# Optimization experiments

Hardware: AMD Instinct MI355X
Metric: run time of the kernel (lower is better)

Reference implementation:

```python
import jax, jax.numpy as jnp
import numpy as np
from jax import lax

PATCH = 15
WIDTH_DCP = 55


def _box_sum(x, r):
    # AvgPool2d(kernel=2r+1, stride=1, padding=r, count_include_pad=True) * (2r+1)^2;
    # the kernel-size factor cancels in all mean_*/N ratios below.
    return lax.reduce_window(x, 0.0, lax.add, (1, 1, 2 * r + 1, 2 * r + 1),
                             (1, 1, 1, 1), ((0, 0), (0, 0), (r, r), (r, r)))


def _guided_filter(I, p, r, eps):
    Nn = _box_sum(jnp.ones_like(p), r)
    mean_I = _box_sum(I, r) / Nn
    mean_p = _box_sum(p, r) / Nn
    mean_Ip = _box_sum(I * p, r) / Nn
    cov_Ip = mean_Ip - mean_I * mean_p
    mean_II = _box_sum(I * I, r) / Nn
    var_I = mean_II - mean_I * mean_I
    a = cov_Ip / (var_I + eps)
    b = mean_p - a * mean_I
    mean_a = _box_sum(a, r) / Nn
    mean_b = _box_sum(b, r) / Nn
    return mean_a * I + mean_b


def _dark_channel(x):
    d = x.min(axis=1, keepdims=True)
    pad = WIDTH_DCP // 2
    d = jnp.pad(d, ((0, 0), (0, 0), (pad, pad), (pad, pad)), constant_values=1.0)
    return lax.reduce_window(d, jnp.inf, lax.min, (1, 1, WIDTH_DCP, WIDTH_DCP),
                             (1, 1, 1, 1), 'VALID')


def _map_A(x):
    N, C, H, W = x.shape
    dc = _dark_channel(x).reshape(N, -1)
    k = int(H * W * 0.001)
    _, idx = lax.top_k(dc, k)  # brightest dark-channel pixels
    xr = x.reshape(N, 3, -1)
    searched = jnp.take_along_axis(xr, jnp.broadcast_to(idx[:, None, :], (N, 3, k)), axis=2)
    A = searched.mean(axis=2)
    return jnp.broadcast_to(A[:, :, None, None], x.shape)


def _t_bccr(haze, mapA, ps):
    t1 = (mapA - haze) / (mapA - 20.0 / 255.0)
    t2 = (mapA - haze) / (mapA - 300.0 / 255.0)
    t = jnp.maximum(t1, t2).max(axis=1, keepdims=True)
    pad = ps // 2
    t = jnp.pad(t, ((0, 0), (0, 0), (pad, pad), (pad, pad)), constant_values=0.0)
    t = lax.reduce_window(t, -jnp.inf, lax.max, (1, 1, ps, ps), (1, 1, 1, 1), 'VALID')
    return jnp.clip(t, 0.05, 1.0)


def _pad_reshape(data, ps):
    N, C, H, W = data.shape
    pad_H = (ps - H % ps) % ps
    pad_W = (ps - W % ps) % ps
    padded = jnp.pad(data, ((0, 0), (0, 0), (pad_H // 2, pad_H - pad_H // 2),
                            (pad_W // 2, pad_W - pad_W // 2)), mode='edge')
    nH = padded.shape[2] // ps
    nW = padded.shape[3] // ps
    p = padded[:, 0].reshape(N, nH, ps, nW, ps).transpose(0, 1, 3, 2, 4)
    p = p.reshape(N, nH * nW, ps * ps).transpose(0, 2, 1)  # [N, ps*ps, P]
    return p, pad_H // 2, pad_W // 2, nH, nW


def _transmission(S, V1, ps, pixel_number=10, slp_length=0.1):
    X, sH, sW, nH, nW = _pad_reshape(V1, ps)  # [N, pp, P]
    Y, _, _, _, _ = _pad_reshape(S, ps)
    dX = X[:, :, None, :] - X[:, None, :, :]          # [N, pp, pp, P]
    dY = Y[:, :, None, :] - Y[:, None, :, :]
    slope = dY / (dX + 1e-8)
    smask = ((slope > -1) & (slope < 0)).astype(X.dtype)
    scount = smask.sum(axis=2)                         # [N, pp, P]
    pmask = (scount >= 0.5 * ps * ps).astype(X.dtype)
    pcount = pmask.sum(axis=1, keepdims=True)          # [N, 1, P]
    mx = (X * pmask).sum(axis=1, keepdims=True) / (pcount + 1e-5)
    my = (Y * pmask).sum(axis=1, keepdims=True) / (pcount + 1e-5)
    k = ((X * Y * pmask).sum(axis=1, keepdims=True) - pcount * mx * my) / (
        ((X * pmask) ** 2).sum(axis=1, keepdims=True) - pcount * mx ** 2 + 1e-5)
    b = my - k * mx
    t = 1.0 + k / (b + 1e-8)
    length = (1.0 + k ** 2) ** 0.5 * ((X * pmask).max(axis=1, keepdims=True)
                                      - (X + 1e8 * (1.0 - pmask)).min(axis=1, keepdims=True))
    tmask = ((pcount > pixel_number) & (length > slp_length) & (k > -1) & (k < 0)
             & (t > 0.01) & (t < 1 - 0.01)).astype(X.dtype)
    t = (t * tmask).reshape(-1, 1, nH, nW)
    t = jnp.repeat(jnp.repeat(t, ps, axis=2), ps, axis=3)  # nearest upsample x ps
    return t[:, :, sH:S.shape[2] + sH, sW:S.shape[3] + sW]


def _percentile(t, bili=0.05):
    N = t.shape[0]
    flat = jnp.where(t > 0, t, 10.0).reshape(N, -1)
    s = jnp.sort(flat, axis=1)
    n = flat.shape[1]
    idx = min(int(bili * n), n - 1)
    return s[:, idx].reshape(-1, 1, 1, 1)


def _restore(image, ps=PATCH):
    mapA = _map_A(image)
    norm = image / mapA
    mx = norm.max(axis=1, keepdims=True)
    S = 1.0 - norm.min(axis=1, keepdims=True) / (mx + 1e-8)
    V1 = 1.0 / (mx + 1e-8)
    t1 = _transmission(S, V1, ps)
    half = ps // 2
    t2 = _transmission(S[:, :, half:, half:], V1[:, :, half:, half:], ps)
    t2 = jnp.pad(t2, ((0, 0), (0, 0), (half, 0), (half, 0)), constant_values=0.0)
    t_slp = jnp.where((t1 != 0) & (t2 != 0), (t1 + t2) / 2.0,
                      jnp.where(t1 != 0, t1, t2))
    t_bl = _t_bccr(image, mapA, ps)
    t_min = _percentile(t_slp)
    t_fusion = jnp.clip(jnp.where(t_slp > 0, t_slp, t_bl), t_min, 1.0)
    t_ref = _guided_filter(image.mean(axis=1, keepdims=True), t_fusion, 2 * ps, 1e-3)
    return (image - mapA) / t_ref + mapA


def setup_inputs() -> dict:
    key = jax.random.key(0)
    image = jax.random.uniform(key, (1, 3, 480, 480), dtype=jnp.float32)
    return {"image": image}


def reference(image):
    return _restore(image)
```

## Files before the change

### kernel.cpp

```cpp
#include <hip/hip_runtime.h>
#include <math.h>

#define W 480
#define HT 480
#define HW (W*HT)
#define GE (HW/256)
#define PP 225
#define NPATCH 1024
#define EQCAP 8192

struct State {
  unsigned slotP[4];
  unsigned slotK[4];
  float sumA[3];
  unsigned eqCount;
  float A[3];
  unsigned tminbits;
  unsigned eqIdx[EQCAP];
  float tp1[NPATCH];
  float tp2[NPATCH];
};

__device__ __forceinline__ void resolve_level(const unsigned* __restrict__ h,
                                              unsigned k_in, int desc,
                                              unsigned* lds,
                                              unsigned& chosen, unsigned& k_out) {
  int t = threadIdx.x;
  unsigned c = h[desc ? (255 - t) : t];
  lds[t] = c;
  __syncthreads();
  for (int s = 1; s < 256; s <<= 1) {
    unsigned add = (t >= s) ? lds[t - s] : 0u;
    __syncthreads();
    lds[t] += add;
    __syncthreads();
  }
  unsigned incl = lds[t];
  unsigned excl = incl - c;
  if (incl >= k_in && excl < k_in) { lds[256] = (unsigned)t; lds[257] = k_in - excl; }
  __syncthreads();
  unsigned tt = lds[256];
  k_out = lds[257];
  chosen = desc ? (255u - tt) : tt;
  __syncthreads();
}

__global__ __launch_bounds__(512) void k_rowmin(const float* __restrict__ img,
                                                float* __restrict__ rowmin,
                                                State* st, unsigned* __restrict__ hist16) {
  __shared__ float l[534];
  int y = blockIdx.x, t = threadIdx.x;
  int g = y * 512 + t;
  if (g < 65536) hist16[g] = 0u;
  for (int i = t; i < 534; i += 512) {
    int col = i - 27;
    float v = 1.0f;
    if ((unsigned)col < (unsigned)W) {
      int q = y * W + col;
      v = fminf(fminf(img[q], img[HW + q]), img[2 * HW + q]);
    }
    l[i] = v;
  }
  if (g == 0) { st->sumA[0] = 0.f; st->sumA[1] = 0.f; st->sumA[2] = 0.f; st->eqCount = 0u; }
  __syncthreads();
  if (t < W) {
    float m = l[t];
    for (int d = 1; d < 55; ++d) m = fminf(m, l[t + d]);
    rowmin[y * W + t] = m;
  }
}

__global__ __launch_bounds__(256) void k_minV3(const float* __restrict__ rowmin,
                                               float* __restrict__ dc,
                                               unsigned* __restrict__ hist16) {
  __shared__ unsigned short bs[256];
  int t = threadIdx.x;
  int p = blockIdx.x * 256 + t;
  int y = p / W, x = p - y * W;
  int lo = y - 27, hi = y + 27;
  float m = (lo < 0 || hi >= HT) ? 1.0f : INFINITY;
  int lo2 = max(lo, 0), hi2 = min(hi, HT - 1);
  for (int yy = lo2; yy <= hi2; ++yy) m = fminf(m, rowmin[yy * W + x]);
  dc[p] = m;
  unsigned b16 = __float_as_uint(m) >> 16;
  bs[t] = (unsigned short)b16;
  __syncthreads();
  int firstIdx = 256, cnt = 0;
  for (int j = 0; j < 256; ++j) {
    if ((unsigned)bs[j] == b16) { ++cnt; if (j < firstIdx) firstIdx = j; }
  }
  if (firstIdx == t) atomicAdd(&hist16[b16], (unsigned)cnt);
}

__global__ __launch_bounds__(256) void k_resolve16(const unsigned* __restrict__ hist16,
                                                   State* st) {
  __shared__ unsigned lds[258];
  __shared__ unsigned lh[256];
  int t = threadIdx.x;
  const uint4* h4 = (const uint4*)hist16;
  unsigned s = 0;
  for (int i = 0; i < 64; ++i) { uint4 v = h4[t * 64 + i]; s += v.x + v.y + v.z + v.w; }
  lh[t] = s;
  __syncthreads();
  unsigned ct, kc;
  resolve_level(lh, 230u, 1, lds, ct, kc);
  lh[t] = hist16[ct * 256 + t];
  __syncthreads();
  unsigned b, kp;
  resolve_level(lh, kc, 1, lds, b, kp);
  if (t == 0) { st->slotP[0] = (ct << 8) | b; st->slotK[0] = kp; }
}

__global__ __launch_bounds__(256) void k_gather2(const float* __restrict__ dc,
                                                 const float* __restrict__ img, State* st) {
  __shared__ float ls[3];
  __shared__ unsigned lcnt, lbase;
  int t = threadIdx.x;
  if (t == 0) { ls[0] = 0.f; ls[1] = 0.f; ls[2] = 0.f; lcnt = 0u; }
  __syncthreads();
  int p = blockIdx.x * 256 + t;
  unsigned p16 = st->slotP[0];
  unsigned b16 = __float_as_uint(dc[p]) >> 16;
  bool eq = (b16 == p16);
  unsigned my = 0;
  if (b16 > p16) {
    atomicAdd(&ls[0], img[p]);
    atomicAdd(&ls[1], img[HW + p]);
    atomicAdd(&ls[2], img[2 * HW + p]);
  } else if (eq) {
    my = atomicAdd(&lcnt, 1u);
  }
  __syncthreads();
  if (t == 0 && lcnt) lbase = atomicAdd(&st->eqCount, lcnt);
  __syncthreads();
  if (eq) { unsigned pos = lbase + my; if (pos < (unsigned)EQCAP) st->eqIdx[pos] = (unsigned)p; }
  if (t == 0 && (ls[0] != 0.f || ls[1] != 0.f || ls[2] != 0.f)) {
    atomicAdd(&st->sumA[0], ls[0]);
    atomicAdd(&st->sumA[1], ls[1]);
    atomicAdd(&st->sumA[2], ls[2]);
  }
}

__global__ __launch_bounds__(256) void k_finalizeA2(const float* __restrict__ dc,
                                                    const float* __restrict__ img, State* st) {
  __shared__ unsigned lds[258];
  __shared__ unsigned lh[256];
  __shared__ unsigned sIdx[EQCAP];
  __shared__ unsigned short sVal[EQCAP];
  __shared__ float ssum[3];
  int t = threadIdx.x;
  unsigned k = st->slotK[0];
  unsigned ne = st->eqCount; if (ne > (unsigned)EQCAP) ne = EQCAP;
  for (int i = t; i < (int)ne; i += 256) {
    unsigned q = st->eqIdx[i];
    sIdx[i] = q;
    sVal[i] = (unsigned short)(__float_as_uint(dc[q]) & 0xFFFFu);
  }
  if (t < 3) ssum[t] = 0.f;
  __syncthreads();
  unsigned vpfx = 0u;
  for (int lev = 0; lev < 2; ++lev) {
    int s = 8 - 8 * lev;
    lh[t] = 0u;
    __syncthreads();
    for (int i = t; i < (int)ne; i += 256) {
      unsigned v = (unsigned)sVal[i];
      if (lev == 0 || (v >> 8) == (vpfx >> 8))
        atomicAdd(&lh[(v >> s) & 0xFFu], 1u);
    }
    __syncthreads();
    unsigned ch, kn;
    resolve_level(lh, k, 1, lds, ch, kn);
    vpfx |= ch << s;
    k = kn;
  }
  unsigned pfx = 0u;
  for (int lev = 0; lev < 3; ++lev) {
    int s = 16 - 8 * lev;
    lh[t] = 0u;
    __syncthreads();
    for (int i = t; i < (int)ne; i += 256) {
      if ((unsigned)sVal[i] == vpfx) {
        unsigned v = sIdx[i];
        if ((v >> (s + 8)) == (pfx >> (s + 8)))
          atomicAdd(&lh[(v >> s) & 0xFFu], 1u);
      }
    }
    __syncthreads();
    unsigned ch, kn;
    resolve_level(lh, k, 0, lds, ch, kn);
    pfx |= ch << s;
    k = kn;
  }
  float a0 = 0.f, a1 = 0.f, a2 = 0.f;
  for (int i = t; i < (int)ne; i += 256) {
    unsigned v = (unsigned)sVal[i], q = sIdx[i];
    if (v > vpfx || (v == vpfx && q <= pfx)) {
      a0 += img[q]; a1 += img[HW + q]; a2 += img[2 * HW + q];
    }
  }
  atomicAdd(&ssum[0], a0); atomicAdd(&ssum[1], a1); atomicAdd(&ssum[2], a2);
  __syncthreads();
  if (t == 0) {
    st->A[0] = (st->sumA[0] + ssum[0]) / 230.0f;
    st->A[1] = (st->sumA[1] + ssum[1]) / 230.0f;
    st->A[2] = (st->sumA[2] + ssum[2]) / 230.0f;
  }
}

__device__ __forceinline__ float wred_sum(float v) { for (int m = 32; m; m >>= 1) v += __shfl_xor(v, m, 64); return v; }
__device__ __forceinline__ float wred_max(float v) { for (int m = 32; m; m >>= 1) v = fmaxf(v, __shfl_xor(v, m, 64)); return v; }
__device__ __forceinline__ float wred_min(float v) { for (int m = 32; m; m >>= 1) v = fminf(v, __shfl_xor(v, m, 64)); return v; }

__global__ __launch_bounds__(256) void k_mega1(const float* __restrict__ img,
                                               float* __restrict__ mh, State* st) {
  __shared__ float2 XY[PP];
  __shared__ float part[4][8];
  __shared__ float Tl[494];
  int b = blockIdx.x;
  int t = threadIdx.x;
  float A0 = st->A[0], A1 = st->A[1], A2 = st->A[2];
  const float c20 = (float)(20.0 / 255.0);
  const float c300 = (float)(300.0 / 255.0);
  if (b >= 2048) {
    int y = b - 2048;
    for (int i = t; i < 494; i += 256) {
      int col = i - 7;
      float v = 0.0f;
      if ((unsigned)col < (unsigned)W) {
        int q = y * W + col;
        float r = img[q], g = img[HW + q], bl = img[2 * HW + q];
        float t0 = fmaxf((A0 - r) / (A0 - c20), (A0 - r) / (A0 - c300));
        float t1 = fmaxf((A1 - g) / (A1 - c20), (A1 - g) / (A1 - c300));
        float t2 = fmaxf((A2 - bl) / (A2 - c20), (A2 - bl) / (A2 - c300));
        v = fmaxf(fmaxf(t0, t1), t2);
      }
      Tl[i] = v;
    }
    __syncthreads();
    for (int x = t; x < W; x += 256) {
      float m = -INFINITY;
      for (int d = 0; d < 15; ++d) m = fmaxf(m, Tl[x + d]);
      mh[y * W + x] = m;
    }
    return;
  }
  int mode = b >> 10;
  int pid = b & 1023;
  int ph = pid >> 5, pw = pid & 31;
  if (t < PP) {
    int r = t / 15, c = t - (t / 15) * 15;
    int y, x;
    if (mode == 0) { y = ph * 15 + r; x = pw * 15 + c; }
    else {
      y = ph * 15 + r + 4; y = (y < 7) ? 7 : ((y > 479) ? 479 : y);
      x = pw * 15 + c + 4; x = (x < 7) ? 7 : ((x > 479) ? 479 : x);
    }
    int q = y * W + x;
    float rr = img[q], gg = img[HW + q], bb = img[2 * HW + q];
    float nr = rr / A0, ng = gg / A1, nb = bb / A2;
    float mx = fmaxf(fmaxf(nr, ng), nb);
    float mn = fminf(fminf(nr, ng), nb);
    float d = mx + 1e-8f;
    XY[t] = make_float2(1.0f / d, 1.0f - mn / d);
  }
  __syncthreads();
  float xi = 0.f, yi = 0.f;
  int cnt = 0;
  if (t < PP) {
    xi = XY[t].x; yi = XY[t].y;
    #pragma unroll 5
    for (int j = 0; j < PP; ++j) {
      float2 o = XY[j];
      float dY = yi - o.y;
      float D = (xi - o.x) + 1e-8f;
      cnt += ((dY * D < 0.0f) && (fabsf(dY) < fabsf(D))) ? 1 : 0;
    }
  }
  float pmf = (t < PP && cnt >= 113) ? 1.0f : 0.0f;
  float xm = xi * pmf, ym = yi * pmf;
  float v0 = wred_sum(pmf);
  float v1 = wred_sum(xm);
  float v2 = wred_sum(ym);
  float v3 = wred_sum(xm * ym);
  float v4 = wred_sum(xm * xm);
  float v5 = wred_max((t < PP) ? xm : -INFINITY);
  float v6 = wred_min((t < PP) ? (xi + 1e8f * (1.0f - pmf)) : INFINITY);
  int wid = t >> 6, lane = t & 63;
  if (lane == 0) {
    part[wid][0] = v0; part[wid][1] = v1; part[wid][2] = v2; part[wid][3] = v3;
    part[wid][4] = v4; part[wid][5] = v5; part[wid][6] = v6;
  }
  __syncthreads();
  if (t == 0) {
    float pcount = 0.f, sx = 0.f, sy = 0.f, sxy = 0.f, sxx = 0.f;
    float mxX = -INFINITY, mnX = INFINITY;
    for (int w2 = 0; w2 < 4; ++w2) {
      pcount += part[w2][0]; sx += part[w2][1]; sy += part[w2][2];
      sxy += part[w2][3]; sxx += part[w2][4];
      mxX = fmaxf(mxX, part[w2][5]); mnX = fminf(mnX, part[w2][6]);
    }
    float den = pcount + 1e-5f;
    float mxv = sx / den, myv = sy / den;
    float kk = (sxy - pcount * mxv * myv) / (sxx - pcount * (mxv * mxv) + 1e-5f);
    float bb = myv - kk * mxv;
    float tt = 1.0f + kk / (bb + 1e-8f);
    float len = sqrtf(1.0f + kk * kk) * (mxX - mnX);
    bool m = (pcount > 10.0f) && (len > 0.1f) && (kk > -1.0f) && (kk < 0.0f)
             && (tt > 0.01f) && (tt < 0.99f);
    float res = tt * (m ? 1.0f : 0.0f);
    if (mode == 0) st->tp1[pid] = res; else st->tp2[pid] = res;
  }
}

__global__ __launch_bounds__(256) void k_maxV_pct(const float* __restrict__ mh,
                                                  float* __restrict__ tb, State* st) {
  __shared__ unsigned lh[256];
  __shared__ unsigned lds[258];
  __shared__ float tp1s[NPATCH], tp2s[NPATCH];
  int b = blockIdx.x;
  int t = threadIdx.x;
  if (b < GE) {
    int p = b * 256 + t;
    int y = p / W, x = p - y * W;
    float m = -INFINITY;
    for (int d = -7; d <= 7; ++d) {
      int yy = y + d;
      float v = ((unsigned)yy < (unsigned)HT) ? mh[yy * W + x] : 0.0f;
      m = fmaxf(m, v);
    }
    tb[p] = fminf(fmaxf(m, 0.05f), 1.0f);
    return;
  }
  for (int i = t; i < NPATCH; i += 256) { tp1s[i] = st->tp1[i]; tp2s[i] = st->tp2[i]; }
  __syncthreads();
  unsigned prefix = 0u, k = 11521u;
  for (int level = 0; level < 4; ++level) {
    lh[t] = 0u;
    __syncthreads();
    unsigned mask = (level == 0) ? 0u : (0xFFFFFFFFu << (32 - 8 * level));
    int shift = 24 - 8 * level;
    for (int i = t; i < NPATCH; i += 256) {
      int ph = i >> 5, pw = i & 31;
      float a = tp1s[i];
      int rcnt[2], ridx[2], ccnt[2], cidx[2];
      if (ph == 0) { rcnt[0] = 7; ridx[0] = -1; rcnt[1] = 8; ridx[1] = 0; }
      else         { rcnt[0] = 4; ridx[0] = ph - 1; rcnt[1] = 11; ridx[1] = ph; }
      if (pw == 0) { ccnt[0] = 7; cidx[0] = -1; ccnt[1] = 8; cidx[1] = 0; }
      else         { ccnt[0] = 4; cidx[0] = pw - 1; ccnt[1] = 11; cidx[1] = pw; }
      for (int ri = 0; ri < 2; ++ri)
        for (int ci = 0; ci < 2; ++ci) {
          unsigned area = (unsigned)(rcnt[ri] * ccnt[ci]);
          float bb = 0.0f;
          if (ridx[ri] >= 0 && cidx[ci] >= 0) bb = tp2s[ridx[ri] * 32 + cidx[ci]];
          float r;
          if (a != 0.0f && bb != 0.0f) r = (a + bb) / 2.0f;
          else r = (a != 0.0f) ? a : bb;
          float u = (r > 0.0f) ? r : 10.0f;
          unsigned bits = __float_as_uint(u);
          if ((bits & mask) == prefix)
            atomicAdd(&lh[(bits >> shift) & 0xFFu], area);
        }
    }
    __syncthreads();
    unsigned ch, kn;
    resolve_level(lh, k, 0, lds, ch, kn);
    prefix |= ch << shift;
    k = kn;
  }
  if (t == 0) st->tminbits = prefix;
}

__global__ __launch_bounds__(512) void k_gf1h(const float* __restrict__ img,
                                              const float* __restrict__ tb,
                                              const State* __restrict__ st,
                                              float4* __restrict__ box4) {
  __shared__ float tp1s[NPATCH], tp2s[NPATCH];
  __shared__ float Pl[540], Il[540];
  int y = blockIdx.x, t = threadIdx.x;
  for (int i = t; i < NPATCH; i += 512) { tp1s[i] = st->tp1[i]; tp2s[i] = st->tp2[i]; }
  __syncthreads();
  float tmin = __uint_as_float(st->tminbits);
  int c1row = (y / 15) * 32;
  bool c2ok = (y >= 7);
  int c2row = c2ok ? ((y - 4) / 15) * 32 : 0;
  for (int i = t; i < 540; i += 512) {
    int col = i - 30;
    float pv = 0.0f, iv = 0.0f;
    if ((unsigned)col < (unsigned)W) {
      int q = y * W + col;
      float a = tp1s[c1row + col / 15];
      float bb = 0.0f;
      if (c2ok && col >= 7) bb = tp2s[c2row + (col - 4) / 15];
      float r;
      if (a != 0.0f && bb != 0.0f) r = (a + bb) / 2.0f;
      else r = (a != 0.0f) ? a : bb;
      float v = (r > 0.0f) ? r : tb[q];
      v = (v < tmin) ? tmin : v;
      v = (v > 1.0f) ? 1.0f : v;
      pv = v;
      iv = ((img[q] + img[HW + q]) + img[2 * HW + q]) / 3.0f;
    }
    Pl[i] = pv; Il[i] = iv;
  }
  __syncthreads();
  if (t < W) {
    float sI = 0.f, sP = 0.f, sIp = 0.f, sII = 0.f;
    for (int d = 0; d < 61; ++d) {
      float iv = Il[t + d], pv = Pl[t + d];
      sI += iv; sP += pv; sIp += iv * pv; sII += iv * iv;
    }
    box4[y * W + t] = make_float4(sI, sP, sIp, sII);
  }
}

__global__ __launch_bounds__(512) void k_gf1vh(const float4* __restrict__ box4,
                                               float2* __restrict__ hab) {
  __shared__ float2 l[540];
  int y = blockIdx.x, t = threadIdx.x;
  float2 v = make_float2(0.f, 0.f);
  if (t < W) {
    float sI = 0.f, sP = 0.f, sIp = 0.f, sII = 0.f;
    for (int d = -30; d <= 30; ++d) {
      int yy = y + d;
      if ((unsigned)yy < (unsigned)HT) {
        float4 b = box4[yy * W + t];
        sI += b.x; sP += b.y; sIp += b.z; sII += b.w;
      }
    }
    int ny = min(y + 30, HT - 1) - max(y - 30, 0) + 1;
    int nx = min(t + 30, W - 1) - max(t - 30, 0) + 1;
    float Nn = (float)(ny * nx);
    float mI = sI / Nn, mP = sP / Nn, mIp = sIp / Nn, mII = sII / Nn;
    float cov = mIp - mI * mP;
    float var = mII - mI * mI;
    float av = cov / (var + 1e-3f);
    v = make_float2(av, mP - av * mI);
  }
  if (t < 30) { l[t] = make_float2(0.f, 0.f); l[510 + t] = make_float2(0.f, 0.f); }
  if (t < W) l[30 + t] = v;
  __syncthreads();
  if (t < W) {
    float sa = 0.f, sb = 0.f;
    for (int d = 0; d < 61; ++d) { float2 u = l[t + d]; sa += u.x; sb += u.y; }
    hab[y * W + t] = make_float2(sa, sb);
  }
}

__global__ __launch_bounds__(256) void k_gf2vfin(const float2* __restrict__ hab,
                                                 const float* __restrict__ img,
                                                 const State* __restrict__ st,
                                                 float* __restrict__ out) {
  int p = blockIdx.x * 256 + threadIdx.x;
  int y = p / W, x = p - y * W;
  float sa = 0.f, sb = 0.f;
  for (int d = -30; d <= 30; ++d) {
    int yy = y + d;
    if ((unsigned)yy < (unsigned)HT) { float2 v = hab[yy * W + x]; sa += v.x; sb += v.y; }
  }
  int ny = min(y + 30, HT - 1) - max(y - 30, 0) + 1;
  int nx = min(x + 30, W - 1) - max(x - 30, 0) + 1;
  float Nn = (float)(ny * nx);
  float r = img[p], g = img[HW + p], bl = img[2 * HW + p];
  float Iv = ((r + g) + bl) / 3.0f;
  float tref = (sa / Nn) * Iv + (sb / Nn);
  float A0 = st->A[0], A1 = st->A[1], A2 = st->A[2];
  out[p]          = (r  - A0) / tref + A0;
  out[HW + p]     = (g  - A1) / tref + A1;
  out[2 * HW + p] = (bl - A2) / tref + A2;
}

extern "C" void kernel_launch(void* const* d_in, const int* in_sizes, int n_in,
                              void* d_out, int out_size, void* d_ws, size_t ws_size,
                              hipStream_t stream) {
  (void)in_sizes; (void)n_in; (void)out_size; (void)ws_size;
  const float* img = (const float*)d_in[0];
  float* out = (float*)d_out;
  State* st = (State*)d_ws;
  unsigned* hist16 = (unsigned*)((char*)d_ws + 65536);
  float* sb = (float*)((char*)d_ws + 65536 + 262144);
  float* bufA = sb;
  float* bufB = sb + HW;
  float4* box4 = (float4*)(sb + 2 * HW);
  float2* hab  = (float2*)(sb + 6 * HW);

  dim3 b256(256), b512(512);
  dim3 ge(GE), rows(HT);

  k_rowmin<<<rows, b512, 0, stream>>>(img, bufB, st, hist16);
  k_minV3<<<ge, b256, 0, stream>>>(bufB, bufA, hist16);
  k_resolve16<<<dim3(1), b256, 0, stream>>>(hist16, st);
  k_gather2<<<ge, b256, 0, stream>>>(bufA, img, st);
  k_finalizeA2<<<dim3(1), b256, 0, stream>>>(bufA, img, st);
  k_mega1<<<dim3(2048 + HT), b256, 0, stream>>>(img, bufB, st);
  k_maxV_pct<<<dim3(GE + 1), b256, 0, stream>>>(bufB, bufA, st);
  k_gf1h<<<rows, b512, 0, stream>>>(img, bufA, st, box4);
  k_gf1vh<<<rows, b512, 0, stream>>>(box4, hab);
  k_gf2vfin<<<ge, b256, 0, stream>>>(hab, img, st, out);
}
```

Measured before the change: 185.5 us.

## Fold single-block resolve kernels into last-block-done tails and fuse vertical max

```diff
diff --git a/kernel.cpp b/kernel.cpp
--- a/kernel.cpp
+++ b/kernel.cpp
@@ -4,7 +4,7 @@
 #define W 480
 #define HT 480
 #define HW (W*HT)
-#define GE (HW/256)
+#define NT (HW/256)
 #define PP 225
 #define NPATCH 1024
 #define EQCAP 8192
@@ -16,6 +16,7 @@
   unsigned eqCount;
   float A[3];
   unsigned tminbits;
+  unsigned done1, done2, done3, pad0;
   unsigned eqIdx[EQCAP];
   float tp1[NPATCH];
   float tp2[NPATCH];
@@ -44,6 +45,10 @@
   chosen = desc ? (255u - tt) : tt;
   __syncthreads();
 }
+
+__device__ __forceinline__ float wred_sum(float v) { for (int m = 32; m; m >>= 1) v += __shfl_xor(v, m, 64); return v; }
+__device__ __forceinline__ float wred_max(float v) { for (int m = 32; m; m >>= 1) v = fmaxf(v, __shfl_xor(v, m, 64)); return v; }
+__device__ __forceinline__ float wred_min(float v) { for (int m = 32; m; m >>= 1) v = fminf(v, __shfl_xor(v, m, 64)); return v; }
 
 __global__ __launch_bounds__(512) void k_rowmin(const float* __restrict__ img,
                                                 float* __restrict__ rowmin,
@@ -61,7 +66,10 @@
     }
     l[i] = v;
   }
-  if (g == 0) { st->sumA[0] = 0.f; st->sumA[1] = 0.f; st->sumA[2] = 0.f; st->eqCount = 0u; }
+  if (g == 0) {
+    st->sumA[0] = 0.f; st->sumA[1] = 0.f; st->sumA[2] = 0.f; st->eqCount = 0u;
+    st->done1 = 0u; st->done2 = 0u; st->done3 = 0u;
+  }
   __syncthreads();
   if (t < W) {
     float m = l[t];
@@ -72,8 +80,11 @@
 
 __global__ __launch_bounds__(256) void k_minV3(const float* __restrict__ rowmin,
                                                float* __restrict__ dc,
-                                               unsigned* __restrict__ hist16) {
+                                               unsigned* __restrict__ hist16, State* st) {
   __shared__ unsigned short bs[256];
+  __shared__ unsigned s_lds[258];
+  __shared__ unsigned s_lh[256];
+  __shared__ unsigned isLast;
   int t = threadIdx.x;
   int p = blockIdx.x * 256 + t;
   int y = p / W, x = p - y * W;
@@ -90,31 +101,39 @@
     if ((unsigned)bs[j] == b16) { ++cnt; if (j < firstIdx) firstIdx = j; }
   }
   if (firstIdx == t) atomicAdd(&hist16[b16], (unsigned)cnt);
-}
-
-__global__ __launch_bounds__(256) void k_resolve16(const unsigned* __restrict__ hist16,
-                                                   State* st) {
-  __shared__ unsigned lds[258];
-  __shared__ unsigned lh[256];
-  int t = threadIdx.x;
-  const uint4* h4 = (const uint4*)hist16;
-  unsigned s = 0;
-  for (int i = 0; i < 64; ++i) { uint4 v = h4[t * 64 + i]; s += v.x + v.y + v.z + v.w; }
-  lh[t] = s;
-  __syncthreads();
-  unsigned ct, kc;
-  resolve_level(lh, 230u, 1, lds, ct, kc);
-  lh[t] = hist16[ct * 256 + t];
-  __syncthreads();
-  unsigned b, kp;
-  resolve_level(lh, kc, 1, lds, b, kp);
-  if (t == 0) { st->slotP[0] = (ct << 8) | b; st->slotK[0] = kp; }
+  if (t == 0) {
+    __threadfence();
+    unsigned old = atomicAdd(&st->done1, 1u);
+    isLast = (old == (unsigned)(NT - 1)) ? 1u : 0u;
+  }
+  __syncthreads();
+  if (isLast) {
+    __threadfence();
+    const uint4* h4 = (const uint4*)hist16;
+    unsigned s = 0;
+    for (int i = 0; i < 64; ++i) { uint4 v = h4[t * 64 + i]; s += v.x + v.y + v.z + v.w; }
+    s_lh[t] = s;
+    __syncthreads();
+    unsigned ct, kc;
+    resolve_level(s_lh, 230u, 1, s_lds, ct, kc);
+    s_lh[t] = hist16[ct * 256 + t];
+    __syncthreads();
+    unsigned b, kp;
+    resolve_level(s_lh, kc, 1, s_lds, b, kp);
+    if (t == 0) { st->slotP[0] = (ct << 8) | b; st->slotK[0] = kp; }
+  }
 }
 
 __global__ __launch_bounds__(256) void k_gather2(const float* __restrict__ dc,
                                                  const float* __restrict__ img, State* st) {
   __shared__ float ls[3];
   __shared__ unsigned lcnt, lbase;
+  __shared__ unsigned isLast;
+  __shared__ unsigned s_lds[258];
+  __shared__ unsigned s_lh[256];
+  __shared__ unsigned sIdx[EQCAP];
+  __shared__ unsigned short sVal[EQCAP];
+  __shared__ float ssum[3];
   int t = threadIdx.x;
   if (t == 0) { ls[0] = 0.f; ls[1] = 0.f; ls[2] = 0.f; lcnt = 0u; }
   __syncthreads();
@@ -139,84 +158,83 @@
     atomicAdd(&st->sumA[1], ls[1]);
     atomicAdd(&st->sumA[2], ls[2]);
   }
-}
-
-__global__ __launch_bounds__(256) void k_finalizeA2(const float* __restrict__ dc,
-                                                    const float* __restrict__ img, State* st) {
-  __shared__ unsigned lds[258];
-  __shared__ unsigned lh[256];
-  __shared__ unsigned sIdx[EQCAP];
-  __shared__ unsigned short sVal[EQCAP];
-  __shared__ float ssum[3];
-  int t = threadIdx.x;
-  unsigned k = st->slotK[0];
-  unsigned ne = st->eqCount; if (ne > (unsigned)EQCAP) ne = EQCAP;
-  for (int i = t; i < (int)ne; i += 256) {
-    unsigned q = st->eqIdx[i];
-    sIdx[i] = q;
-    sVal[i] = (unsigned short)(__float_as_uint(dc[q]) & 0xFFFFu);
-  }
-  if (t < 3) ssum[t] = 0.f;
-  __syncthreads();
-  unsigned vpfx = 0u;
-  for (int lev = 0; lev < 2; ++lev) {
-    int s = 8 - 8 * lev;
-    lh[t] = 0u;
-    __syncthreads();
+  if (t == 0) {
+    __threadfence();
+    unsigned old = atomicAdd(&st->done2, 1u);
+    isLast = (old == (unsigned)(NT - 1)) ? 1u : 0u;
+  }
+  __syncthreads();
+  if (isLast) {
+    __threadfence();
+    unsigned k = st->slotK[0];
+    unsigned ne = st->eqCount; if (ne > (unsigned)EQCAP) ne = EQCAP;
     for (int i = t; i < (int)ne; i += 256) {
-      unsigned v = (unsigned)sVal[i];
-      if (lev == 0 || (v >> 8) == (vpfx >> 8))
-        atomicAdd(&lh[(v >> s) & 0xFFu], 1u);
-    }
-    __syncthreads();
-    unsigned ch, kn;
-    resolve_level(lh, k, 1, lds, ch, kn);
-    vpfx |= ch << s;
-    k = kn;
-  }
-  unsigned pfx = 0u;
-  for (int lev = 0; lev < 3; ++lev) {
-    int s = 16 - 8 * lev;
-    lh[t] = 0u;
-    __syncthreads();
+      unsigned q = st->eqIdx[i];
+      sIdx[i] = q;
+      sVal[i] = (unsigned short)(__float_as_uint(dc[q]) & 0xFFFFu);
+    }
+    if (t < 3) ssum[t] = 0.f;
+    __syncthreads();
+    unsigned vpfx = 0u;
+    for (int lev = 0; lev < 2; ++lev) {
+      int s = 8 - 8 * lev;
+      s_lh[t] = 0u;
+      __syncthreads();
+      for (int i = t; i < (int)ne; i += 256) {
+        unsigned v = (unsigned)sVal[i];
+        if (lev == 0 || (v >> 8) == (vpfx >> 8))
+          atomicAdd(&s_lh[(v >> s) & 0xFFu], 1u);
+      }
+      __syncthreads();
+      unsigned ch, kn;
+      resolve_level(s_lh, k, 1, s_lds, ch, kn);
+      vpfx |= ch << s;
+      k = kn;
+    }
+    unsigned pfx = 0u;
+    for (int lev = 0; lev < 3; ++lev) {
+      int s = 16 - 8 * lev;
+      s_lh[t] = 0u;
+      __syncthreads();
+      for (int i = t; i < (int)ne; i += 256) {
+        if ((unsigned)sVal[i] == vpfx) {
+          unsigned v = sIdx[i];
+          if ((v >> (s + 8)) == (pfx >> (s + 8)))
+            atomicAdd(&s_lh[(v >> s) & 0xFFu], 1u);
+        }
+      }
+      __syncthreads();
+      unsigned ch, kn;
+      resolve_level(s_lh, k, 0, s_lds, ch, kn);
+      pfx |= ch << s;
+      k = kn;
+    }
+    float a0 = 0.f, a1 = 0.f, a2 = 0.f;
     for (int i = t; i < (int)ne; i += 256) {
-      if ((unsigned)sVal[i] == vpfx) {
-        unsigned v = sIdx[i];
-        if ((v >> (s + 8)) == (pfx >> (s + 8)))
-          atomicAdd(&lh[(v >> s) & 0xFFu], 1u);
+      unsigned v = (unsigned)sVal[i], q = sIdx[i];
+      if (v > vpfx || (v == vpfx && q <= pfx)) {
+        a0 += img[q]; a1 += img[HW + q]; a2 += img[2 * HW + q];
       }
     }
-    __syncthreads();
-    unsigned ch, kn;
-    resolve_level(lh, k, 0, lds, ch, kn);
-    pfx |= ch << s;
-    k = kn;
-  }
-  float a0 = 0.f, a1 = 0.f, a2 = 0.f;
-  for (int i = t; i < (int)ne; i += 256) {
-    unsigned v = (unsigned)sVal[i], q = sIdx[i];
-    if (v > vpfx || (v == vpfx && q <= pfx)) {
-      a0 += img[q]; a1 += img[HW + q]; a2 += img[2 * HW + q];
-    }
-  }
-  atomicAdd(&ssum[0], a0); atomicAdd(&ssum[1], a1); atomicAdd(&ssum[2], a2);
-  __syncthreads();
-  if (t == 0) {
-    st->A[0] = (st->sumA[0] + ssum[0]) / 230.0f;
-    st->A[1] = (st->sumA[1] + ssum[1]) / 230.0f;
-    st->A[2] = (st->sumA[2] + ssum[2]) / 230.0f;
-  }
-}
-
-__device__ __forceinline__ float wred_sum(float v) { for (int m = 32; m; m >>= 1) v += __shfl_xor(v, m, 64); return v; }
-__device__ __forceinline__ float wred_max(float v) { for (int m = 32; m; m >>= 1) v = fmaxf(v, __shfl_xor(v, m, 64)); return v; }
-__device__ __forceinline__ float wred_min(float v) { for (int m = 32; m; m >>= 1) v = fminf(v, __shfl_xor(v, m, 64)); return v; }
+    atomicAdd(&ssum[0], a0); atomicAdd(&ssum[1], a1); atomicAdd(&ssum[2], a2);
+    __syncthreads();
+    if (t == 0) {
+      st->A[0] = (st->sumA[0] + ssum[0]) / 230.0f;
+      st->A[1] = (st->sumA[1] + ssum[1]) / 230.0f;
+      st->A[2] = (st->sumA[2] + ssum[2]) / 230.0f;
+    }
+  }
+}
 
 __global__ __launch_bounds__(256) void k_mega1(const float* __restrict__ img,
                                                float* __restrict__ mh, State* st) {
   __shared__ float2 XY[PP];
   __shared__ float part[4][8];
   __shared__ float Tl[494];
+  __shared__ unsigned isLast;
+  __shared__ unsigned s_lds[258];
+  __shared__ unsigned s_lh[256];
+  __shared__ float tp1s[NPATCH], tp2s[NPATCH];
   int b = blockIdx.x;
   int t = threadIdx.x;
   float A0 = st->A[0], A1 = st->A[1], A2 = st->A[2];
@@ -311,74 +329,72 @@
     float res = tt * (m ? 1.0f : 0.0f);
     if (mode == 0) st->tp1[pid] = res; else st->tp2[pid] = res;
   }
-}
-
-__global__ __launch_bounds__(256) void k_maxV_pct(const float* __restrict__ mh,
-                                                  float* __restrict__ tb, State* st) {
-  __shared__ unsigned lh[256];
-  __shared__ unsigned lds[258];
+  if (t == 0) {
+    __threadfence();
+    unsigned old = atomicAdd(&st->done3, 1u);
+    isLast = (old == 2047u) ? 1u : 0u;
+  }
+  __syncthreads();
+  if (isLast) {
+    __threadfence();
+    for (int i = t; i < NPATCH; i += 256) { tp1s[i] = st->tp1[i]; tp2s[i] = st->tp2[i]; }
+    __syncthreads();
+    unsigned prefix = 0u, k = 11521u;
+    for (int level = 0; level < 4; ++level) {
+      s_lh[t] = 0u;
+      __syncthreads();
+      unsigned mask = (level == 0) ? 0u : (0xFFFFFFFFu << (32 - 8 * level));
+      int shift = 24 - 8 * level;
+      for (int i = t; i < NPATCH; i += 256) {
+        int phh = i >> 5, pww = i & 31;
+        float a = tp1s[i];
+        int rcnt[2], ridx[2], ccnt[2], cidx[2];
+        if (phh == 0) { rcnt[0] = 7; ridx[0] = -1; rcnt[1] = 8; ridx[1] = 0; }
+        else          { rcnt[0] = 4; ridx[0] = phh - 1; rcnt[1] = 11; ridx[1] = phh; }
+        if (pww == 0) { ccnt[0] = 7; cidx[0] = -1; ccnt[1] = 8; cidx[1] = 0; }
+        else          { ccnt[0] = 4; cidx[0] = pww - 1; ccnt[1] = 11; cidx[1] = pww; }
+        for (int ri = 0; ri < 2; ++ri)
+          for (int ci = 0; ci < 2; ++ci) {
+            unsigned area = (unsigned)(rcnt[ri] * ccnt[ci]);
+            float bb = 0.0f;
+            if (ridx[ri] >= 0 && cidx[ci] >= 0) bb = tp2s[ridx[ri] * 32 + cidx[ci]];
+            float r;
+            if (a != 0.0f && bb != 0.0f) r = (a + bb) / 2.0f;
+            else r = (a != 0.0f) ? a : bb;
+            float u = (r > 0.0f) ? r : 10.0f;
+            unsigned bits = __float_as_uint(u);
+            if ((bits & mask) == prefix)
+              atomicAdd(&s_lh[(bits >> shift) & 0xFFu], area);
+          }
+      }
+      __syncthreads();
+      unsigned ch, kn;
+      resolve_level(s_lh, k, 0, s_lds, ch, kn);
+      prefix |= ch << shift;
+      k = kn;
+    }
+    if (t == 0) st->tminbits = prefix;
+  }
+}
+
+__global__ __launch_bounds__(512) void k_gf1h(const float* __restrict__ img,
+                                              const float* __restrict__ mh,
+                                              const State* __restrict__ st,
+                                              float4* __restrict__ box4) {
   __shared__ float tp1s[NPATCH], tp2s[NPATCH];
-  int b = blockIdx.x;
-  int t = threadIdx.x;
-  if (b < GE) {
-    int p = b * 256 + t;
-    int y = p / W, x = p - y * W;
+  __shared__ float Pl[540], Il[540];
+  __shared__ float tbv[480];
+  int y = blockIdx.x, t = threadIdx.x;
+  for (int i = t; i < NPATCH; i += 512) { tp1s[i] = st->tp1[i]; tp2s[i] = st->tp2[i]; }
+  for (int x = t; x < W; x += 512) {
     float m = -INFINITY;
     for (int d = -7; d <= 7; ++d) {
       int yy = y + d;
       float v = ((unsigned)yy < (unsigned)HT) ? mh[yy * W + x] : 0.0f;
       m = fmaxf(m, v);
     }
-    tb[p] = fminf(fmaxf(m, 0.05f), 1.0f);
-    return;
-  }
-  for (int i = t; i < NPATCH; i += 256) { tp1s[i] = st->tp1[i]; tp2s[i] = st->tp2[i]; }
-  __syncthreads();
-  unsigned prefix = 0u, k = 11521u;
-  for (int level = 0; level < 4; ++level) {
-    lh[t] = 0u;
-    __syncthreads();
-    unsigned mask = (level == 0) ? 0u : (0xFFFFFFFFu << (32 - 8 * level));
-    int shift = 24 - 8 * level;
-    for (int i = t; i < NPATCH; i += 256) {
-      int ph = i >> 5, pw = i & 31;
-      float a = tp1s[i];
-      int rcnt[2], ridx[2], ccnt[2], cidx[2];
-      if (ph == 0) { rcnt[0] = 7; ridx[0] = -1; rcnt[1] = 8; ridx[1] = 0; }
-      else         { rcnt[0] = 4; ridx[0] = ph - 1; rcnt[1] = 11; ridx[1] = ph; }
-      if (pw == 0) { ccnt[0] = 7; cidx[0] = -1; ccnt[1] = 8; cidx[1] = 0; }
-      else         { ccnt[0] = 4; cidx[0] = pw - 1; ccnt[1] = 11; cidx[1] = pw; }
-      for (int ri = 0; ri < 2; ++ri)
-        for (int ci = 0; ci < 2; ++ci) {
-          unsigned area = (unsigned)(rcnt[ri] * ccnt[ci]);
-          float bb = 0.0f;
-          if (ridx[ri] >= 0 && cidx[ci] >= 0) bb = tp2s[ridx[ri] * 32 + cidx[ci]];
-          float r;
-          if (a != 0.0f && bb != 0.0f) r = (a + bb) / 2.0f;
-          else r = (a != 0.0f) ? a : bb;
-          float u = (r > 0.0f) ? r : 10.0f;
-          unsigned bits = __float_as_uint(u);
-          if ((bits & mask) == prefix)
-            atomicAdd(&lh[(bits >> shift) & 0xFFu], area);
-        }
-    }
-    __syncthreads();
-    unsigned ch, kn;
-    resolve_level(lh, k, 0, lds, ch, kn);
-    prefix |= ch << shift;
-    k = kn;
-  }
-  if (t == 0) st->tminbits = prefix;
-}
-
-__global__ __launch_bounds__(512) void k_gf1h(const float* __restrict__ img,
-                                              const float* __restrict__ tb,
-                                              const State* __restrict__ st,
-                                              float4* __restrict__ box4) {
-  __shared__ float tp1s[NPATCH], tp2s[NPATCH];
-  __shared__ float Pl[540], Il[540];
-  int y = blockIdx.x, t = threadIdx.x;
-  for (int i = t; i < NPATCH; i += 512) { tp1s[i] = st->tp1[i]; tp2s[i] = st->tp2[i]; }
+    tbv[x] = fminf(fmaxf(m, 0.05f), 1.0f);
+  }
   __syncthreads();
   float tmin = __uint_as_float(st->tminbits);
   int c1row = (y / 15) * 32;
@@ -395,7 +411,7 @@
       float r;
       if (a != 0.0f && bb != 0.0f) r = (a + bb) / 2.0f;
       else r = (a != 0.0f) ? a : bb;
-      float v = (r > 0.0f) ? r : tb[q];
+      float v = (r > 0.0f) ? r : tbv[col];
       v = (v < tmin) ? tmin : v;
       v = (v > 1.0f) ? 1.0f : v;
       pv = v;
@@ -485,16 +501,13 @@
   float2* hab  = (float2*)(sb + 6 * HW);
 
   dim3 b256(256), b512(512);
-  dim3 ge(GE), rows(HT);
+  dim3 ge(NT), rows(HT);
 
   k_rowmin<<<rows, b512, 0, stream>>>(img, bufB, st, hist16);
-  k_minV3<<<ge, b256, 0, stream>>>(bufB, bufA, hist16);
-  k_resolve16<<<dim3(1), b256, 0, stream>>>(hist16, st);
+  k_minV3<<<ge, b256, 0, stream>>>(bufB, bufA, hist16, st);
   k_gather2<<<ge, b256, 0, stream>>>(bufA, img, st);
-  k_finalizeA2<<<dim3(1), b256, 0, stream>>>(bufA, img, st);
   k_mega1<<<dim3(2048 + HT), b256, 0, stream>>>(img, bufB, st);
-  k_maxV_pct<<<dim3(GE + 1), b256, 0, stream>>>(bufB, bufA, st);
-  k_gf1h<<<rows, b512, 0, stream>>>(img, bufA, st, box4);
+  k_gf1h<<<rows, b512, 0, stream>>>(img, bufB, st, box4);
   k_gf1vh<<<rows, b512, 0, stream>>>(box4, hab);
   k_gf2vfin<<<ge, b256, 0, stream>>>(hab, img, st, out);
 }
```

After: 227.7 us. 22.7% more time.

## Fuse vertical max filter into guided-filter row kernel and vectorize SLP pair test

Applied to the files above, without the earlier changes.

```diff
diff --git a/kernel.cpp b/kernel.cpp
--- a/kernel.cpp
+++ b/kernel.cpp
@@ -4,7 +4,7 @@
 #define W 480
 #define HT 480
 #define HW (W*HT)
-#define GE (HW/256)
+#define NT (HW/256)
 #define PP 225
 #define NPATCH 1024
 #define EQCAP 8192
@@ -44,6 +44,10 @@
   chosen = desc ? (255u - tt) : tt;
   __syncthreads();
 }
+
+__device__ __forceinline__ float wred_sum(float v) { for (int m = 32; m; m >>= 1) v += __shfl_xor(v, m, 64); return v; }
+__device__ __forceinline__ float wred_max(float v) { for (int m = 32; m; m >>= 1) v = fmaxf(v, __shfl_xor(v, m, 64)); return v; }
+__device__ __forceinline__ float wred_min(float v) { for (int m = 32; m; m >>= 1) v = fminf(v, __shfl_xor(v, m, 64)); return v; }
 
 __global__ __launch_bounds__(512) void k_rowmin(const float* __restrict__ img,
                                                 float* __restrict__ rowmin,
@@ -208,13 +212,13 @@
   }
 }
 
-__device__ __forceinline__ float wred_sum(float v) { for (int m = 32; m; m >>= 1) v += __shfl_xor(v, m, 64); return v; }
-__device__ __forceinline__ float wred_max(float v) { for (int m = 32; m; m >>= 1) v = fmaxf(v, __shfl_xor(v, m, 64)); return v; }
-__device__ __forceinline__ float wred_min(float v) { for (int m = 32; m; m >>= 1) v = fminf(v, __shfl_xor(v, m, 64)); return v; }
+#define SLPTEST(ox, oy) \
+  ((((yi - (oy)) * ((xi - (ox)) + 1e-8f)) < 0.0f) && \
+   (fabsf(yi - (oy)) < fabsf((xi - (ox)) + 1e-8f)) ? 1 : 0)
 
 __global__ __launch_bounds__(256) void k_mega1(const float* __restrict__ img,
                                                float* __restrict__ mh, State* st) {
-  __shared__ float2 XY[PP];
+  __shared__ __align__(16) float2 XY[PP + 1];
   __shared__ float part[4][8];
   __shared__ float Tl[494];
   int b = blockIdx.x;
@@ -269,13 +273,21 @@
   int cnt = 0;
   if (t < PP) {
     xi = XY[t].x; yi = XY[t].y;
-    #pragma unroll 5
-    for (int j = 0; j < PP; ++j) {
-      float2 o = XY[j];
-      float dY = yi - o.y;
-      float D = (xi - o.x) + 1e-8f;
-      cnt += ((dY * D < 0.0f) && (fabsf(dY) < fabsf(D))) ? 1 : 0;
-    }
+    const float4* XY4 = (const float4*)XY;
+    int c0 = 0, c1 = 0, c2 = 0, c3 = 0;
+    #pragma unroll 2
+    for (int j4 = 0; j4 < 112; j4 += 4) {
+      float4 a = XY4[j4 + 0];
+      float4 bq = XY4[j4 + 1];
+      float4 cq = XY4[j4 + 2];
+      float4 dq = XY4[j4 + 3];
+      c0 += SLPTEST(a.x, a.y);   c1 += SLPTEST(a.z, a.w);
+      c2 += SLPTEST(bq.x, bq.y); c3 += SLPTEST(bq.z, bq.w);
+      c0 += SLPTEST(cq.x, cq.y); c1 += SLPTEST(cq.z, cq.w);
+      c2 += SLPTEST(dq.x, dq.y); c3 += SLPTEST(dq.z, dq.w);
+    }
+    { float2 o = XY[224]; c0 += SLPTEST(o.x, o.y); }
+    cnt = (c0 + c1) + (c2 + c3);
   }
   float pmf = (t < PP && cnt >= 113) ? 1.0f : 0.0f;
   float xm = xi * pmf, ym = yi * pmf;
@@ -313,25 +325,11 @@
   }
 }
 
-__global__ __launch_bounds__(256) void k_maxV_pct(const float* __restrict__ mh,
-                                                  float* __restrict__ tb, State* st) {
+__global__ __launch_bounds__(256) void k_pct(State* st) {
   __shared__ unsigned lh[256];
   __shared__ unsigned lds[258];
   __shared__ float tp1s[NPATCH], tp2s[NPATCH];
-  int b = blockIdx.x;
-  int t = threadIdx.x;
-  if (b < GE) {
-    int p = b * 256 + t;
-    int y = p / W, x = p - y * W;
-    float m = -INFINITY;
-    for (int d = -7; d <= 7; ++d) {
-      int yy = y + d;
-      float v = ((unsigned)yy < (unsigned)HT) ? mh[yy * W + x] : 0.0f;
-      m = fmaxf(m, v);
-    }
-    tb[p] = fminf(fmaxf(m, 0.05f), 1.0f);
-    return;
-  }
+  int t = threadIdx.x;
   for (int i = t; i < NPATCH; i += 256) { tp1s[i] = st->tp1[i]; tp2s[i] = st->tp2[i]; }
   __syncthreads();
   unsigned prefix = 0u, k = 11521u;
@@ -372,13 +370,23 @@
 }
 
 __global__ __launch_bounds__(512) void k_gf1h(const float* __restrict__ img,
-                                              const float* __restrict__ tb,
+                                              const float* __restrict__ mh,
                                               const State* __restrict__ st,
                                               float4* __restrict__ box4) {
   __shared__ float tp1s[NPATCH], tp2s[NPATCH];
   __shared__ float Pl[540], Il[540];
+  __shared__ float tbv[480];
   int y = blockIdx.x, t = threadIdx.x;
   for (int i = t; i < NPATCH; i += 512) { tp1s[i] = st->tp1[i]; tp2s[i] = st->tp2[i]; }
+  for (int x = t; x < W; x += 512) {
+    float m = -INFINITY;
+    for (int d = -7; d <= 7; ++d) {
+      int yy = y + d;
+      float v = ((unsigned)yy < (unsigned)HT) ? mh[yy * W + x] : 0.0f;
+      m = fmaxf(m, v);
+    }
+    tbv[x] = fminf(fmaxf(m, 0.05f), 1.0f);
+  }
   __syncthreads();
   float tmin = __uint_as_float(st->tminbits);
   int c1row = (y / 15) * 32;
@@ -395,7 +403,7 @@
       float r;
       if (a != 0.0f && bb != 0.0f) r = (a + bb) / 2.0f;
       else r = (a != 0.0f) ? a : bb;
-      float v = (r > 0.0f) ? r : tb[q];
+      float v = (r > 0.0f) ? r : tbv[col];
       v = (v < tmin) ? tmin : v;
       v = (v > 1.0f) ? 1.0f : v;
       pv = v;
@@ -485,7 +493,7 @@
   float2* hab  = (float2*)(sb + 6 * HW);
 
   dim3 b256(256), b512(512);
-  dim3 ge(GE), rows(HT);
+  dim3 ge(NT), rows(HT);
 
   k_rowmin<<<rows, b512, 0, stream>>>(img, bufB, st, hist16);
   k_minV3<<<ge, b256, 0, stream>>>(bufB, bufA, hist16);
@@ -493,8 +501,8 @@
   k_gather2<<<ge, b256, 0, stream>>>(bufA, img, st);
   k_finalizeA2<<<dim3(1), b256, 0, stream>>>(bufA, img, st);
   k_mega1<<<dim3(2048 + HT), b256, 0, stream>>>(img, bufB, st);
-  k_maxV_pct<<<dim3(GE + 1), b256, 0, stream>>>(bufB, bufA, st);
-  k_gf1h<<<rows, b512, 0, stream>>>(img, bufA, st, box4);
+  k_pct<<<dim3(1), b256, 0, stream>>>(st);
+  k_gf1h<<<rows, b512, 0, stream>>>(img, bufB, st, box4);
   k_gf1vh<<<rows, b512, 0, stream>>>(box4, hab);
   k_gf2vfin<<<ge, b256, 0, stream>>>(hab, img, st, out);
 }
```

New measurement: 186.9 us. Within noise of the previous version (+0.7%).
